# Performance work log

Measured on AMD Instinct MI355X. Metric: run time of the kernel, lower is better.

Reference implementation:

```python
import jax, jax.numpy as jnp
import numpy as np

B, T, D, H = 4, 4096, 1024, 64

def setup_inputs() -> dict:
    key = jax.random.key(0)
    k1, k2, k3, k4 = jax.random.split(key, 4)
    scale = 1.0 / np.sqrt(D)
    return {
        "x": jax.random.normal(k1, (B, T, D), dtype=jnp.float32),
        "Wq": jax.random.normal(k2, (D, H), dtype=jnp.float32) * scale,
        "Wk": jax.random.normal(k3, (D, H), dtype=jnp.float32) * scale,
        "Wv": jax.random.normal(k4, (D, H), dtype=jnp.float32) * scale,
    }

def reference(x, Wq, Wk, Wv):
    # Projections (Linear without bias): [B,T,H]
    q = jnp.einsum('btd,dh->bth', x, Wq)
    k = jnp.einsum('btd,dh->bth', x, Wk)
    v = jnp.einsum('btd,dh->bth', x, Wv)
    head_size = q.shape[-1]
    # Full T x T scores, scaled by sqrt(head_size) as in the source
    attn = jnp.einsum('bqh,bkh->bqk', q, k) / jnp.sqrt(jnp.float32(head_size))
    t = x.shape[1]
    causal = jnp.tril(jnp.ones((t, t), dtype=bool))  # [T,T]
    attn = jnp.where(causal[None, :, :], attn, -jnp.inf)
    attn = jax.nn.softmax(attn, axis=-1)
    # dropout prob = 0.0 -> identity
    out = jnp.einsum('bqk,bkh->bqh', attn, v)
    return out
```

## Files before the change

kernel.cpp:

```cpp
#include <hip/hip_runtime.h>
#include <hip/hip_bf16.h>
#include <math.h>

#define BB 4
#define TT 4096
#define DD 1024
#define HH 64
#define MTOT (BB * TT)
#define NCH 4
#define LD 72
#define LDP 136

typedef short short8 __attribute__((ext_vector_type(8)));
typedef float f32x4  __attribute__((ext_vector_type(4)));
typedef unsigned int u32;

__device__ __forceinline__ unsigned short f2bf(float f) {
    unsigned u = __builtin_bit_cast(unsigned, f);
    unsigned r = (u + 0x7fffu + ((u >> 16) & 1u)) >> 16;
    return (unsigned short)r;
}

__device__ __forceinline__ unsigned long long pack4(float a, float b, float c, float d) {
    return (unsigned long long)f2bf(a) |
           ((unsigned long long)f2bf(b) << 16) |
           ((unsigned long long)f2bf(c) << 32) |
           ((unsigned long long)f2bf(d) << 48);
}

__device__ __forceinline__ short8 pack8(float4 a, float4 b) {
    short8 r;
    r[0] = (short)f2bf(a.x); r[1] = (short)f2bf(a.y);
    r[2] = (short)f2bf(a.z); r[3] = (short)f2bf(a.w);
    r[4] = (short)f2bf(b.x); r[5] = (short)f2bf(b.y);
    r[6] = (short)f2bf(b.z); r[7] = (short)f2bf(b.w);
    return r;
}

__device__ __forceinline__ void gl16(const void* g, void* l) {
    __builtin_amdgcn_global_load_lds(
        (const __attribute__((address_space(1))) u32*)g,
        (__attribute__((address_space(3))) u32*)l, 16, 0, 0);
}

#define QOFF  0
#define KOFF  (MTOT * HH)
#define VOFF  (2 * MTOT * HH)
#define BF_TOTAL (3 * MTOT * HH)

__global__ __launch_bounds__(256) void transpose_w(
    const float* __restrict__ Wq, const float* __restrict__ Wk,
    const float* __restrict__ Wv, unsigned short* __restrict__ Wt)
{
    const int w = blockIdx.y;
    const float* W = (w == 0) ? Wq : (w == 1) ? Wk : Wv;
    unsigned short* o = Wt + (size_t)w * 64 * 1024;
    const int t  = threadIdx.x;
    const int n4 = t & 15;
    const int k0 = blockIdx.x * 64 + (t >> 4) * 4;

    float v[4][4];
#pragma unroll
    for (int ii = 0; ii < 4; ++ii) {
        float4 r = *(const float4*)&W[(size_t)(k0 + ii) * HH + n4 * 4];
        v[ii][0] = r.x; v[ii][1] = r.y; v[ii][2] = r.z; v[ii][3] = r.w;
    }
#pragma unroll
    for (int cc = 0; cc < 4; ++cc) {
        unsigned long long pk = pack4(v[0][cc], v[1][cc], v[2][cc], v[3][cc]);
        *(unsigned long long*)&o[(size_t)(n4 * 4 + cc) * 1024 + k0] = pk;
    }
}

__global__ __launch_bounds__(256, 2) void qkv_proj(
    const float* __restrict__ x,
    const unsigned short* __restrict__ Wt,
    unsigned short* __restrict__ qkv)
{
    const int tid   = threadIdx.x;
    const int lane  = tid & 63;
    const int wave  = tid >> 6;
    const int l15   = lane & 15;
    const int quad  = lane >> 4;
    const int m0    = blockIdx.x * 32;
    const int strip = wave & 1;
    const int half  = wave >> 1;

    __shared__ float          Af[2][32 * 64];
    __shared__ unsigned short Bs[2][192 * 64];

    const int ar  = lane >> 4;
    const int as  = lane & 15;
    const int bc  = lane >> 3;
    const int bs2 = (lane & 7) ^ bc;

#define STAGE(it, p)                                                         \
    {                                                                        \
        const int kc_ = (it) * 64;                                           \
        _Pragma("unroll")                                                    \
        for (int jj = 0; jj < 2; ++jj) {                                     \
            int j   = wave * 2 + jj;                                         \
            int row = 4 * j + ar;                                            \
            int sw  = as ^ (row & 15);                                       \
            gl16(x + (size_t)(m0 + row) * DD + kc_ + sw * 4,                 \
                 &Af[p][j * 256]);                                           \
        }                                                                    \
        _Pragma("unroll")                                                    \
        for (int jj = 0; jj < 6; ++jj) {                                     \
            int j    = wave * 6 + jj;                                        \
            int gcol = 8 * j + bc;                                           \
            gl16(Wt + (size_t)gcol * 1024 + kc_ + bs2 * 8,                   \
                 &Bs[p][j * 512]);                                           \
        }                                                                    \
    }

    f32x4 acc[6];
#pragma unroll
    for (int i = 0; i < 6; ++i) acc[i] = (f32x4){0.f, 0.f, 0.f, 0.f};

    STAGE(0, 0)
    __syncthreads();
    int p = 0;

    for (int it = 0; it < 16; ++it) {
        if (it < 15) STAGE(it + 1, p ^ 1)

        const int row = strip * 16 + l15;
#pragma unroll
        for (int ks = 0; ks < 2; ++ks) {
            int c0 = ks * 8 + quad * 2;
            float4 a0 = *(const float4*)&Af[p][row * 64 + ((c0)     ^ l15) * 4];
            float4 a1 = *(const float4*)&Af[p][row * 64 + ((c0 + 1) ^ l15) * 4];
            short8 af = pack8(a0, a1);
            int cb = (ks * 4 + quad) ^ (l15 & 7);
#pragma unroll
            for (int jj = 0; jj < 6; ++jj) {
                int col = (half * 6 + jj) * 16 + l15;
                short8 bfr = *(const short8*)&Bs[p][col * 64 + cb * 8];
                acc[jj] = __builtin_amdgcn_mfma_f32_16x16x32_bf16(af, bfr, acc[jj], 0, 0, 0);
            }
        }
        __syncthreads();
        p ^= 1;
    }
#undef STAGE

    const float QS = 0.125f * 1.44269504088896f;
    unsigned short* q_bf  = qkv + QOFF;
    unsigned short* k_bf  = qkv + KOFF;
    unsigned short* vt_bf = qkv + VOFF;
#pragma unroll
    for (int jj = 0; jj < 6; ++jj) {
        int g = half * 6 + jj, w = g >> 2, col = (g & 3) * 16 + l15;
#pragma unroll
        for (int r = 0; r < 4; ++r) {
            int m = m0 + strip * 16 + quad * 4 + r;
            float val = acc[jj][r];
            if (w == 0) val *= QS;
            unsigned short bv = f2bf(val);
            if (w == 0)      q_bf[(size_t)m * HH + col] = bv;
            else if (w == 1) k_bf[(size_t)m * HH + col] = bv;
            else {
                int b = m >> 12, t = m & 4095;
                vt_bf[(size_t)b * HH * TT + (size_t)col * TT + t] = bv;
            }
        }
    }
}

__global__ __launch_bounds__(256, 3) void flash_attn(
    const unsigned short* __restrict__ qkv,
    float* __restrict__ Opart,
    float* __restrict__ Mpart,
    float* __restrict__ Lpart)
{
    const int qt = 63 - blockIdx.x;
    const int b  = blockIdx.y;
    const int c  = blockIdx.z;
    if (c * 16 > qt) return;
    const int j0   = c * 16;
    const int jmax = min(j0 + 16, qt + 1);

    const int tid  = threadIdx.x;
    const int lane = tid & 63;
    const int wave = tid >> 6;
    const int l15  = lane & 15;
    const int quad = lane >> 4;

    const unsigned short* q_g  = qkv + QOFF + (size_t)b * TT * HH;
    const unsigned short* k_g  = qkv + KOFF + (size_t)b * TT * HH;
    const unsigned short* vt_g = qkv + VOFF + (size_t)b * HH * TT;

    __shared__ unsigned short Ks[128 * LD];
    __shared__ unsigned short Vs[64 * 136];
    __shared__ unsigned short Ps[4 * 16 * LDP];
    unsigned short* Pw = Ps + wave * 16 * LDP;

    short8 qf[2];
#pragma unroll
    for (int kk = 0; kk < 2; ++kk)
        qf[kk] = *(const short8*)&q_g[(size_t)(qt * 64 + wave * 16 + l15) * HH + kk * 32 + quad * 8];

    f32x4 ov[4];
#pragma unroll
    for (int i = 0; i < 4; ++i) ov[i] = (f32x4){0.f, 0.f, 0.f, 0.f};
    float m_run = -1e30f, l_run = 0.f;

    const int srow = tid >> 3;
    const int seg  = tid & 7;

    ulonglong2 kreg[4], vreg[4];

#define LOADR(jr_)                                                            \
    {                                                                         \
        const unsigned short* kp = k_g  + (size_t)(jr_) * 64 * HH;            \
        const unsigned short* vp = vt_g + (size_t)(jr_) * 64;                 \
        _Pragma("unroll")                                                     \
        for (int r4 = 0; r4 < 4; ++r4)                                        \
            kreg[r4] = *(const ulonglong2*)&kp[(size_t)(srow + r4 * 32) * HH + seg * 8]; \
        _Pragma("unroll")                                                     \
        for (int c2 = 0; c2 < 2; ++c2)                                        \
            _Pragma("unroll")                                                 \
            for (int r2 = 0; r2 < 2; ++r2)                                    \
                vreg[c2 * 2 + r2] = *(const ulonglong2*)&vp[(size_t)(srow + r2 * 32) * TT + (seg + c2 * 8) * 8]; \
    }

    LOADR(j0)

    for (int jr = j0; jr < jmax; jr += 2) {
        const bool two = (jmax - jr) >= 2;

        __syncthreads();
#pragma unroll
        for (int r4 = 0; r4 < 4; ++r4)
            *(ulonglong2*)&Ks[(srow + r4 * 32) * LD + seg * 8] = kreg[r4];
#pragma unroll
        for (int c2 = 0; c2 < 2; ++c2)
#pragma unroll
            for (int r2 = 0; r2 < 2; ++r2)
                *(ulonglong2*)&Vs[(srow + r2 * 32) * 136 + (seg + c2 * 8) * 8] = vreg[c2 * 2 + r2];
        __syncthreads();

        if (jr + 2 < jmax) LOADR(jr + 2)

        f32x4 st0[4], st1[4];
#pragma unroll
        for (int i = 0; i < 4; ++i) {
            st0[i] = (f32x4){0.f, 0.f, 0.f, 0.f};
            st1[i] = (f32x4){0.f, 0.f, 0.f, 0.f};
        }
#pragma unroll
        for (int kk = 0; kk < 2; ++kk)
#pragma unroll
            for (int mt = 0; mt < 4; ++mt) {
                short8 a = *(const short8*)&Ks[(mt * 16 + l15) * LD + kk * 32 + quad * 8];
                st0[mt] = __builtin_amdgcn_mfma_f32_16x16x32_bf16(a, qf[kk], st0[mt], 0, 0, 0);
            }
        if (two) {
#pragma unroll
            for (int kk = 0; kk < 2; ++kk)
#pragma unroll
                for (int mt = 0; mt < 4; ++mt) {
                    short8 a = *(const short8*)&Ks[(64 + mt * 16 + l15) * LD + kk * 32 + quad * 8];
                    st1[mt] = __builtin_amdgcn_mfma_f32_16x16x32_bf16(a, qf[kk], st1[mt], 0, 0, 0);
                }
        }

        const int qg = wave * 16 + l15;
        if (jr == qt) {
#pragma unroll
            for (int mt = 0; mt < 4; ++mt)
#pragma unroll
                for (int r = 0; r < 4; ++r)
                    if (mt * 16 + quad * 4 + r > qg) st0[mt][r] = -1e30f;
        } else if (two && jr + 1 == qt) {
#pragma unroll
            for (int mt = 0; mt < 4; ++mt)
#pragma unroll
                for (int r = 0; r < 4; ++r)
                    if (mt * 16 + quad * 4 + r > qg) st1[mt][r] = -1e30f;
        }

        float mloc = -1e30f;
#pragma unroll
        for (int mt = 0; mt < 4; ++mt)
#pragma unroll
            for (int r = 0; r < 4; ++r) mloc = fmaxf(mloc, st0[mt][r]);
        if (two) {
#pragma unroll
            for (int mt = 0; mt < 4; ++mt)
#pragma unroll
                for (int r = 0; r < 4; ++r) mloc = fmaxf(mloc, st1[mt][r]);
        }
        mloc = fmaxf(mloc, __shfl_xor(mloc, 16));
        mloc = fmaxf(mloc, __shfl_xor(mloc, 32));
        const float m_new = fmaxf(m_run, mloc);
        const float alpha = exp2f(m_run - m_new);
        m_run = m_new;

        float ssum = 0.f;
#pragma unroll
        for (int mt = 0; mt < 4; ++mt)
#pragma unroll
            for (int r = 0; r < 4; ++r) {
                float pv = exp2f(st0[mt][r] - m_new);
                st0[mt][r] = pv; ssum += pv;
            }
        if (two) {
#pragma unroll
            for (int mt = 0; mt < 4; ++mt)
#pragma unroll
                for (int r = 0; r < 4; ++r) {
                    float pv = exp2f(st1[mt][r] - m_new);
                    st1[mt][r] = pv; ssum += pv;
                }
        }
        ssum += __shfl_xor(ssum, 16);
        ssum += __shfl_xor(ssum, 32);
        l_run = l_run * alpha + ssum;

#pragma unroll
        for (int mt = 0; mt < 4; ++mt) {
            u32 p0, p1;
            asm("v_cvt_pk_bf16_f32 %0, %1, %2" : "=v"(p0) : "v"(st0[mt][0]), "v"(st0[mt][1]));
            asm("v_cvt_pk_bf16_f32 %0, %1, %2" : "=v"(p1) : "v"(st0[mt][2]), "v"(st0[mt][3]));
            uint2 pr; pr.x = p0; pr.y = p1;
            *(uint2*)&Pw[l15 * LDP + mt * 16 + quad * 4] = pr;
        }
        if (two) {
#pragma unroll
            for (int mt = 0; mt < 4; ++mt) {
                u32 p0, p1;
                asm("v_cvt_pk_bf16_f32 %0, %1, %2" : "=v"(p0) : "v"(st1[mt][0]), "v"(st1[mt][1]));
                asm("v_cvt_pk_bf16_f32 %0, %1, %2" : "=v"(p1) : "v"(st1[mt][2]), "v"(st1[mt][3]));
                uint2 pr; pr.x = p0; pr.y = p1;
                *(uint2*)&Pw[l15 * LDP + 64 + mt * 16 + quad * 4] = pr;
            }
        }

        {
            float a0 = __shfl(alpha, quad * 4 + 0);
            float a1 = __shfl(alpha, quad * 4 + 1);
            float a2 = __shfl(alpha, quad * 4 + 2);
            float a3 = __shfl(alpha, quad * 4 + 3);
#pragma unroll
            for (int ht = 0; ht < 4; ++ht) {
                ov[ht][0] *= a0; ov[ht][1] *= a1;
                ov[ht][2] *= a2; ov[ht][3] *= a3;
            }
        }
#pragma unroll
        for (int kk = 0; kk < 2; ++kk) {
            short8 a = *(const short8*)&Pw[l15 * LDP + kk * 32 + quad * 8];
#pragma unroll
            for (int ht = 0; ht < 4; ++ht) {
                short8 bf = *(const short8*)&Vs[(ht * 16 + l15) * 136 + kk * 32 + quad * 8];
                ov[ht] = __builtin_amdgcn_mfma_f32_16x16x32_bf16(a, bf, ov[ht], 0, 0, 0);
            }
        }
        if (two) {
#pragma unroll
            for (int kk = 0; kk < 2; ++kk) {
                short8 a = *(const short8*)&Pw[l15 * LDP + 64 + kk * 32 + quad * 8];
#pragma unroll
                for (int ht = 0; ht < 4; ++ht) {
                    short8 bf = *(const short8*)&Vs[(ht * 16 + l15) * 136 + 64 + kk * 32 + quad * 8];
                    ov[ht] = __builtin_amdgcn_mfma_f32_16x16x32_bf16(a, bf, ov[ht], 0, 0, 0);
                }
            }
        }
    }
#undef LOADR

    float* Ob = Opart + ((size_t)((b * 64 + qt) * NCH + c)) * 4096;
#pragma unroll
    for (int ht = 0; ht < 4; ++ht)
#pragma unroll
        for (int r = 0; r < 4; ++r)
            Ob[(size_t)(wave * 16 + quad * 4 + r) * HH + ht * 16 + l15] = ov[ht][r];
    if (quad == 0) {
        size_t mi = (size_t)((b * 64 + qt) * NCH + c) * 64 + wave * 16 + l15;
        Mpart[mi] = m_run;
        Lpart[mi] = l_run;
    }
}

__global__ __launch_bounds__(256) void combine(
    const float* __restrict__ Opart,
    const float* __restrict__ Mpart,
    const float* __restrict__ Lpart,
    float* __restrict__ out)
{
    const int qt = blockIdx.x;
    const int b  = blockIdx.y;
    const int nc = (qt >> 4) + 1;
    const int t  = threadIdx.x;
    const int row = t >> 2;
    const int seg = t & 3;

    const size_t base = (size_t)(b * 64 + qt) * NCH;

    float m_c[NCH], M = -1e30f;
    for (int c = 0; c < nc; ++c) {
        m_c[c] = Mpart[(base + c) * 64 + row];
        M = fmaxf(M, m_c[c]);
    }
    float L = 0.f, w_c[NCH];
    for (int c = 0; c < nc; ++c) {
        w_c[c] = exp2f(m_c[c] - M);
        L += w_c[c] * Lpart[(base + c) * 64 + row];
    }
    float invL = 1.0f / L;

    f32x4 o[4];
#pragma unroll
    for (int i = 0; i < 4; ++i) o[i] = (f32x4){0.f, 0.f, 0.f, 0.f};
    for (int c = 0; c < nc; ++c) {
        const float* Ob = Opart + (base + c) * 4096 + (size_t)row * HH + seg * 16;
#pragma unroll
        for (int i = 0; i < 4; ++i) {
            f32x4 v = *(const f32x4*)(Ob + i * 4);
            o[i] += v * w_c[c];
        }
    }
    float* op = out + ((size_t)b * TT + qt * 64 + row) * HH + seg * 16;
#pragma unroll
    for (int i = 0; i < 4; ++i)
        *(f32x4*)(op + i * 4) = o[i] * invL;
}

extern "C" void kernel_launch(void* const* d_in, const int* in_sizes, int n_in,
                              void* d_out, int out_size, void* d_ws, size_t ws_size,
                              hipStream_t stream) {
    const float* x  = (const float*)d_in[0];
    const float* Wq = (const float*)d_in[1];
    const float* Wk = (const float*)d_in[2];
    const float* Wv = (const float*)d_in[3];
    float* out = (float*)d_out;

    unsigned short* qkv = (unsigned short*)d_ws;
    float* Opart = (float*)((char*)d_ws + BF_TOTAL * 2);
    float* Mpart = Opart + (size_t)BB * 64 * NCH * 4096;
    float* Lpart = Mpart + (size_t)BB * 64 * NCH * 64;

    unsigned short* Wt = (unsigned short*)d_out;

    transpose_w<<<dim3(16, 3), 256, 0, stream>>>(Wq, Wk, Wv, Wt);
    qkv_proj<<<dim3(MTOT / 32), 256, 0, stream>>>(x, Wt, qkv);
    flash_attn<<<dim3(64, BB, NCH), 256, 0, stream>>>(qkv, Opart, Mpart, Lpart);
    combine<<<dim3(64, BB), 256, 0, stream>>>(Opart, Mpart, Lpart, out);
}
```

Baseline: 190.2 us.

## Double-buffer K/V tiles in LDS via direct global-to-LDS loads in attention

The attention kernel no longer loads K/V into registers and then writes them to padded LDS. It now uses gl16 direct global-to-LDS copies into double-buffered, XOR-swizzled LDS tiles, prefetching the next tile during compute, which removes one of the two barriers per iteration. The P buffer shrinks to a 64-column tile that is reused for each half of the pair, and the occupancy hint of 3 blocks is dropped from launch_bounds. The cost is doubled K/V LDS usage (about 73KB total), which may limit occupancy.

```diff
diff --git a/kernel.cpp b/kernel.cpp
--- a/kernel.cpp
+++ b/kernel.cpp
@@ -8,8 +8,6 @@
 #define HH 64
 #define MTOT (BB * TT)
 #define NCH 4
-#define LD 72
-#define LDP 136
 
 typedef short short8 __attribute__((ext_vector_type(8)));
 typedef float f32x4  __attribute__((ext_vector_type(4)));
@@ -94,7 +92,7 @@
     const int bc  = lane >> 3;
     const int bs2 = (lane & 7) ^ bc;
 
-#define STAGE(it, p)                                                         \
+#define STAGEW(it, p)                                                        \
     {                                                                        \
         const int kc_ = (it) * 64;                                           \
         _Pragma("unroll")                                                    \
@@ -118,12 +116,12 @@
 #pragma unroll
     for (int i = 0; i < 6; ++i) acc[i] = (f32x4){0.f, 0.f, 0.f, 0.f};
 
-    STAGE(0, 0)
+    STAGEW(0, 0)
     __syncthreads();
     int p = 0;
 
     for (int it = 0; it < 16; ++it) {
-        if (it < 15) STAGE(it + 1, p ^ 1)
+        if (it < 15) STAGEW(it + 1, p ^ 1)
 
         const int row = strip * 16 + l15;
 #pragma unroll
@@ -143,7 +141,7 @@
         __syncthreads();
         p ^= 1;
     }
-#undef STAGE
+#undef STAGEW
 
     const float QS = 0.125f * 1.44269504088896f;
     unsigned short* q_bf  = qkv + QOFF;
@@ -168,7 +166,7 @@
     }
 }
 
-__global__ __launch_bounds__(256, 3) void flash_attn(
+__global__ __launch_bounds__(256) void flash_attn(
     const unsigned short* __restrict__ qkv,
     float* __restrict__ Opart,
     float* __restrict__ Mpart,
@@ -191,57 +189,53 @@
     const unsigned short* k_g  = qkv + KOFF + (size_t)b * TT * HH;
     const unsigned short* vt_g = qkv + VOFF + (size_t)b * HH * TT;
 
-    __shared__ unsigned short Ks[128 * LD];
-    __shared__ unsigned short Vs[64 * 136];
-    __shared__ unsigned short Ps[4 * 16 * LDP];
-    unsigned short* Pw = Ps + wave * 16 * LDP;
-
-    short8 qf[2];
-#pragma unroll
-    for (int kk = 0; kk < 2; ++kk)
-        qf[kk] = *(const short8*)&q_g[(size_t)(qt * 64 + wave * 16 + l15) * HH + kk * 32 + quad * 8];
-
-    f32x4 ov[4];
-#pragma unroll
-    for (int i = 0; i < 4; ++i) ov[i] = (f32x4){0.f, 0.f, 0.f, 0.f};
-    float m_run = -1e30f, l_run = 0.f;
-
-    const int srow = tid >> 3;
-    const int seg  = tid & 7;
-
-    ulonglong2 kreg[4], vreg[4];
-
-#define LOADR(jr_)                                                            \
+    __shared__ unsigned short Ks[2][128 * 64];
+    __shared__ unsigned short Vs[2][64 * 128];
+    __shared__ unsigned short Ps[4][16 * 72];
+    unsigned short* Pw = &Ps[wave][0];
+
+    const int kr3 = lane >> 3;
+    const int kch = lane & 7;
+    const int vr2 = lane >> 4;
+    const int vch = lane & 15;
+
+#define STAGE(jr_, p_)                                                        \
     {                                                                         \
         const unsigned short* kp = k_g  + (size_t)(jr_) * 64 * HH;            \
         const unsigned short* vp = vt_g + (size_t)(jr_) * 64;                 \
         _Pragma("unroll")                                                     \
-        for (int r4 = 0; r4 < 4; ++r4)                                        \
-            kreg[r4] = *(const ulonglong2*)&kp[(size_t)(srow + r4 * 32) * HH + seg * 8]; \
+        for (int i = 0; i < 4; ++i) {                                         \
+            int g = wave * 4 + i;                                             \
+            gl16(kp + (size_t)(g * 8 + kr3) * HH + (kch ^ kr3) * 8,           \
+                 &Ks[p_][g * 512]);                                           \
+        }                                                                     \
         _Pragma("unroll")                                                     \
-        for (int c2 = 0; c2 < 2; ++c2)                                        \
-            _Pragma("unroll")                                                 \
-            for (int r2 = 0; r2 < 2; ++r2)                                    \
-                vreg[c2 * 2 + r2] = *(const ulonglong2*)&vp[(size_t)(srow + r2 * 32) * TT + (seg + c2 * 8) * 8]; \
-    }
-
-    LOADR(j0)
+        for (int i = 0; i < 4; ++i) {                                         \
+            int g = wave * 4 + i;                                             \
+            int h = g * 4 + vr2;                                              \
+            gl16(vp + (size_t)h * TT + (vch ^ (h & 15)) * 8,                  \
+                 &Vs[p_][g * 512]);                                           \
+        }                                                                     \
+    }
+
+    short8 qf[2];
+#pragma unroll
+    for (int kk = 0; kk < 2; ++kk)
+        qf[kk] = *(const short8*)&q_g[(size_t)(qt * 64 + wave * 16 + l15) * HH + kk * 32 + quad * 8];
+
+    f32x4 ov[4];
+#pragma unroll
+    for (int i = 0; i < 4; ++i) ov[i] = (f32x4){0.f, 0.f, 0.f, 0.f};
+    float m_run = -1e30f, l_run = 0.f;
+
+    STAGE(j0, 0)
+    __syncthreads();
+    int p = 0;
 
     for (int jr = j0; jr < jmax; jr += 2) {
         const bool two = (jmax - jr) >= 2;
 
-        __syncthreads();
-#pragma unroll
-        for (int r4 = 0; r4 < 4; ++r4)
-            *(ulonglong2*)&Ks[(srow + r4 * 32) * LD + seg * 8] = kreg[r4];
-#pragma unroll
-        for (int c2 = 0; c2 < 2; ++c2)
-#pragma unroll
-            for (int r2 = 0; r2 < 2; ++r2)
-                *(ulonglong2*)&Vs[(srow + r2 * 32) * 136 + (seg + c2 * 8) * 8] = vreg[c2 * 2 + r2];
-        __syncthreads();
-
-        if (jr + 2 < jmax) LOADR(jr + 2)
+        if (jr + 2 < jmax) STAGE(jr + 2, p ^ 1)
 
         f32x4 st0[4], st1[4];
 #pragma unroll
@@ -253,7 +247,8 @@
         for (int kk = 0; kk < 2; ++kk)
 #pragma unroll
             for (int mt = 0; mt < 4; ++mt) {
-                short8 a = *(const short8*)&Ks[(mt * 16 + l15) * LD + kk * 32 + quad * 8];
+                short8 a = *(const short8*)&Ks[p][(mt * 16 + l15) * 64 +
+                                                  (((kk * 4 + quad) ^ (l15 & 7)) * 8)];
                 st0[mt] = __builtin_amdgcn_mfma_f32_16x16x32_bf16(a, qf[kk], st0[mt], 0, 0, 0);
             }
         if (two) {
@@ -261,7 +256,8 @@
             for (int kk = 0; kk < 2; ++kk)
 #pragma unroll
                 for (int mt = 0; mt < 4; ++mt) {
-                    short8 a = *(const short8*)&Ks[(64 + mt * 16 + l15) * LD + kk * 32 + quad * 8];
+                    short8 a = *(const short8*)&Ks[p][(64 + mt * 16 + l15) * 64 +
+                                                      (((kk * 4 + quad) ^ (l15 & 7)) * 8)];
                     st1[mt] = __builtin_amdgcn_mfma_f32_16x16x32_bf16(a, qf[kk], st1[mt], 0, 0, 0);
                 }
         }
@@ -319,14 +315,37 @@
         ssum += __shfl_xor(ssum, 32);
         l_run = l_run * alpha + ssum;
 
+        {
+            float a0 = __shfl(alpha, quad * 4 + 0);
+            float a1 = __shfl(alpha, quad * 4 + 1);
+            float a2 = __shfl(alpha, quad * 4 + 2);
+            float a3 = __shfl(alpha, quad * 4 + 3);
+#pragma unroll
+            for (int ht = 0; ht < 4; ++ht) {
+                ov[ht][0] *= a0; ov[ht][1] *= a1;
+                ov[ht][2] *= a2; ov[ht][3] *= a3;
+            }
+        }
+
 #pragma unroll
         for (int mt = 0; mt < 4; ++mt) {
             u32 p0, p1;
             asm("v_cvt_pk_bf16_f32 %0, %1, %2" : "=v"(p0) : "v"(st0[mt][0]), "v"(st0[mt][1]));
             asm("v_cvt_pk_bf16_f32 %0, %1, %2" : "=v"(p1) : "v"(st0[mt][2]), "v"(st0[mt][3]));
             uint2 pr; pr.x = p0; pr.y = p1;
-            *(uint2*)&Pw[l15 * LDP + mt * 16 + quad * 4] = pr;
-        }
+            *(uint2*)&Pw[l15 * 72 + mt * 16 + quad * 4] = pr;
+        }
+#pragma unroll
+        for (int kk = 0; kk < 2; ++kk) {
+            short8 a = *(const short8*)&Pw[l15 * 72 + kk * 32 + quad * 8];
+#pragma unroll
+            for (int ht = 0; ht < 4; ++ht) {
+                short8 bf = *(const short8*)&Vs[p][(ht * 16 + l15) * 128 +
+                                                   (((kk * 4 + quad) ^ l15) * 8)];
+                ov[ht] = __builtin_amdgcn_mfma_f32_16x16x32_bf16(a, bf, ov[ht], 0, 0, 0);
+            }
+        }
+
         if (two) {
 #pragma unroll
             for (int mt = 0; mt < 4; ++mt) {
@@ -334,43 +353,24 @@
                 asm("v_cvt_pk_bf16_f32 %0, %1, %2" : "=v"(p0) : "v"(st1[mt][0]), "v"(st1[mt][1]));
                 asm("v_cvt_pk_bf16_f32 %0, %1, %2" : "=v"(p1) : "v"(st1[mt][2]), "v"(st1[mt][3]));
                 uint2 pr; pr.x = p0; pr.y = p1;
-                *(uint2*)&Pw[l15 * LDP + 64 + mt * 16 + quad * 4] = pr;
-            }
-        }
-
-        {
-            float a0 = __shfl(alpha, quad * 4 + 0);
-            float a1 = __shfl(alpha, quad * 4 + 1);
-            float a2 = __shfl(alpha, quad * 4 + 2);
-            float a3 = __shfl(alpha, quad * 4 + 3);
-#pragma unroll
-            for (int ht = 0; ht < 4; ++ht) {
-                ov[ht][0] *= a0; ov[ht][1] *= a1;
-                ov[ht][2] *= a2; ov[ht][3] *= a3;
-            }
-        }
-#pragma unroll
-        for (int kk = 0; kk < 2; ++kk) {
-            short8 a = *(const short8*)&Pw[l15 * LDP + kk * 32 + quad * 8];
-#pragma unroll
-            for (int ht = 0; ht < 4; ++ht) {
-                short8 bf = *(const short8*)&Vs[(ht * 16 + l15) * 136 + kk * 32 + quad * 8];
-                ov[ht] = __builtin_amdgcn_mfma_f32_16x16x32_bf16(a, bf, ov[ht], 0, 0, 0);
-            }
-        }
-        if (two) {
+                *(uint2*)&Pw[l15 * 72 + mt * 16 + quad * 4] = pr;
+            }
 #pragma unroll
             for (int kk = 0; kk < 2; ++kk) {
-                short8 a = *(const short8*)&Pw[l15 * LDP + 64 + kk * 32 + quad * 8];
+                short8 a = *(const short8*)&Pw[l15 * 72 + kk * 32 + quad * 8];
 #pragma unroll
                 for (int ht = 0; ht < 4; ++ht) {
-                    short8 bf = *(const short8*)&Vs[(ht * 16 + l15) * 136 + 64 + kk * 32 + quad * 8];
+                    short8 bf = *(const short8*)&Vs[p][(ht * 16 + l15) * 128 +
+                                                       (((8 + kk * 4 + quad) ^ l15) * 8)];
                     ov[ht] = __builtin_amdgcn_mfma_f32_16x16x32_bf16(a, bf, ov[ht], 0, 0, 0);
                 }
             }
         }
-    }
-#undef LOADR
+
+        __syncthreads();
+        p ^= 1;
+    }
+#undef STAGE
 
     float* Ob = Opart + ((size_t)((b * 64 + qt) * NCH + c)) * 4096;
 #pragma unroll
```

After: 163.0 us. 14.3% less time.
